# Kernel tuning notes

Hardware: AMD Instinct MI355X
Metric: run time of the kernel (lower is better)

## Reference

```python
import jax, jax.numpy as jnp
import numpy as np

B, S, E = 2, 2048, 4096
HQ, HKV, D = 32, 8, 128
WINDOW = 1024
SOFT_CAP = 50.0
Q_PRE_ATTN = 128.0
TT_SCALE = 0.1
TT_FLOOR = 8192.0
EPS = 1e-6
ROPE_BASE = 10000.0


def l2norm(x):
    return x * jax.lax.rsqrt(jnp.mean(x * x, axis=-1, keepdims=True) + EPS)


def apply_rope(x, pos):
    # x: [B,S,H,D]; half-split rotary, base 10000
    half = x.shape[-1] // 2
    freq = ROPE_BASE ** (-jnp.arange(half, dtype=jnp.float32) * 2.0 / x.shape[-1])  # [half]
    angle = pos.astype(jnp.float32)[:, None] * freq[None, :]                         # [S,half]
    cos = jnp.cos(angle)[None, :, None, :]
    sin = jnp.sin(angle)[None, :, None, :]
    x1, x2 = x[..., :half], x[..., half:]
    return jnp.concatenate([x1 * cos - x2 * sin, x2 * cos + x1 * sin], axis=-1)


def setup_inputs() -> dict:
    key = jax.random.key(0)
    ks = jax.random.split(key, 5)
    sc = 0.02
    return {
        "x": jax.random.normal(ks[0], (B, S, E), jnp.float32),
        "Wq": jax.random.normal(ks[1], (E, HQ, D), jnp.float32) * sc,
        "Wk": jax.random.normal(ks[2], (E, HKV, D), jnp.float32) * sc,
        "Wv": jax.random.normal(ks[3], (E, HKV, D), jnp.float32) * sc,
        "Wo": jax.random.normal(ks[4], (HQ, D, E), jnp.float32) * sc,
    }


def reference(x, Wq, Wk, Wv, Wo):
    pos = jnp.arange(S)
    # QKV projections
    q = jnp.einsum('bse,ehd->bshd', x, Wq)   # [B,S,HQ,D]
    k = jnp.einsum('bse,ehd->bshd', x, Wk)   # [B,S,HKV,D]
    v = jnp.einsum('bse,ehd->bshd', x, Wv)   # [B,S,HKV,D]
    # QK norm (L2Norm) then RoPE
    q = apply_rope(l2norm(q), pos)
    k = apply_rope(l2norm(k), pos)
    # query pre-attention scaling
    q = q * (Q_PRE_ATTN ** -0.5)
    # temperature tuning: per-position scale
    attn_scale = jnp.log(jnp.floor((pos.astype(jnp.float32) + 1.0) / TT_FLOOR) + 1.0) * TT_SCALE + 1.0
    q = q * attn_scale[None, :, None, None]
    # GQA: expand kv heads
    g = HQ // HKV
    k_r = jnp.repeat(k, g, axis=2)           # [B,S,HQ,D]
    v_r = jnp.repeat(v, g, axis=2)
    logits = jnp.einsum('bihd,bjhd->bhij', q, k_r).astype(jnp.float32)
    # tanh soft cap
    logits = SOFT_CAP * jnp.tanh(logits / SOFT_CAP)
    # causal + sliding window mask: j <= i and i - j < WINDOW
    i = pos[:, None]
    j = pos[None, :]
    mask = (j <= i) & ((i - j) < WINDOW)     # [S,S]
    logits = jnp.where(mask[None, None], logits, jnp.float32(-1e30))
    probs = jax.nn.softmax(logits, axis=-1)
    out = jnp.einsum('bhij,bjhd->bihd', probs, v_r)  # [B,S,HQ,D]
    return jnp.einsum('bihd,hde->bie', out, Wo)      # [B,S,E]
```

## Files before the change

### kernel.cpp

```cpp
#include <hip/hip_runtime.h>


typedef unsigned short u16;
typedef unsigned int   u32;
typedef __bf16 bf16x8 __attribute__((ext_vector_type(8)));
typedef float  f32x4  __attribute__((ext_vector_type(4)));

typedef __attribute__((address_space(1))) void* gas_ptr;
typedef __attribute__((address_space(3))) void* las_ptr;

__device__ __forceinline__ void load_lds16(const void* g, void* l) {
  __builtin_amdgcn_global_load_lds((gas_ptr)g, (las_ptr)l, 16, 0, 0);
}

__device__ __forceinline__ u16 f2bf(float f) {
  u32 u = __builtin_bit_cast(u32, f);
  u += 0x7fffu + ((u >> 16) & 1u);
  return (u16)(u >> 16);
}
__device__ __forceinline__ float bf2f(u16 h) {
  u32 u = ((u32)h) << 16;
  return __builtin_bit_cast(float, u);
}
__device__ __forceinline__ u32 pack_trunc(float a, float b) {
  return (__builtin_bit_cast(u32, a) >> 16) | (__builtin_bit_cast(u32, b) & 0xffff0000u);
}

__global__ __launch_bounds__(256) void cast_f32_bf16(const float* __restrict__ src,
                                                     u16* __restrict__ dst) {
  size_t i = ((size_t)blockIdx.x * 256 + threadIdx.x) * 8;
  float4 a = *(const float4*)(src + i);
  float4 b = *(const float4*)(src + i + 4);
  uint4 o;
  o.x = (u32)f2bf(a.x) | ((u32)f2bf(a.y) << 16);
  o.y = (u32)f2bf(a.z) | ((u32)f2bf(a.w) << 16);
  o.z = (u32)f2bf(b.x) | ((u32)f2bf(b.y) << 16);
  o.w = (u32)f2bf(b.z) | ((u32)f2bf(b.w) << 16);
  *(uint4*)(dst + i) = o;
}

__global__ __launch_bounds__(256) void transpose_cast_f32_bf16(
    const float* __restrict__ src, u16* __restrict__ dst, int R, int C) {
  __shared__ float tile[32][33];
  const int tx = threadIdx.x & 31, ty = threadIdx.x >> 5;
  const int r0 = blockIdx.y * 32, c0 = blockIdx.x * 32;
#pragma unroll
  for (int i = 0; i < 4; ++i)
    tile[ty + i * 8][tx] = src[(size_t)(r0 + ty + i * 8) * C + (c0 + tx)];
  __syncthreads();
#pragma unroll
  for (int i = 0; i < 4; ++i)
    dst[(size_t)(c0 + ty + i * 8) * R + (r0 + tx)] = f2bf(tile[tx][ty + i * 8]);
}

__global__ __launch_bounds__(256) void transpose_v(const u16* __restrict__ src,
                                                   u16* __restrict__ dst) {
  __shared__ u16 tile[32][34];
  const int plane = blockIdx.z;
  const u16* s = src + (size_t)plane * 2048 * 128;
  u16* d = dst + (size_t)plane * 2048 * 128;
  const int tx = threadIdx.x & 31, ty = threadIdx.x >> 5;
  const int r0 = blockIdx.x * 32, c0 = blockIdx.y * 32;
#pragma unroll
  for (int i = 0; i < 4; ++i)
    tile[ty + i * 8][tx] = s[(size_t)(r0 + ty + i * 8) * 128 + (c0 + tx)];
  __syncthreads();
#pragma unroll
  for (int i = 0; i < 4; ++i)
    d[(size_t)(c0 + ty + i * 8) * 2048 + (r0 + tx)] = tile[tx][ty + i * 8];
}

template <int OUT_BF16>
__global__ __launch_bounds__(256) void gemm_bt(const u16* __restrict__ A,
                                               const u16* __restrict__ Bt,
                                               void* __restrict__ Cout,
                                               int M, int N, int K) {
  __shared__ __align__(16) u16 As[128 * 32];
  __shared__ __align__(16) u16 Bs[128 * 32];
  const int t = threadIdx.x;
  const int lane = t & 63, w = t >> 6;
  const int c = lane & 15, quad = lane >> 4;
  const int m0 = blockIdx.y * 128, n0 = blockIdx.x * 128;
  const int wm = (w >> 1) * 64, wn = (w & 1) * 64;
  const int srow = lane >> 2;
  const int sch = ((lane & 3) ^ ((lane >> 3) & 3)) * 8;

  f32x4 acc[4][4];
#pragma unroll
  for (int i = 0; i < 4; ++i)
#pragma unroll
    for (int j = 0; j < 4; ++j)
#pragma unroll
      for (int r = 0; r < 4; ++r) acc[i][j][r] = 0.0f;

  const u16* Ab = A + (size_t)(m0 + w * 16 + srow) * K + sch;
  const u16* Bb = Bt + (size_t)(n0 + w * 16 + srow) * K + sch;
  const size_t row64 = (size_t)64 * K;
  u16* AsW = &As[(w * 16) * 32];
  u16* AsW2 = &As[(64 + w * 16) * 32];
  u16* BsW = &Bs[(w * 16) * 32];
  u16* BsW2 = &Bs[(64 + w * 16) * 32];

  for (int k0 = 0; k0 < K; k0 += 32) {
    __syncthreads();
    load_lds16(Ab + k0, AsW);
    load_lds16(Ab + row64 + k0, AsW2);
    load_lds16(Bb + k0, BsW);
    load_lds16(Bb + row64 + k0, BsW2);
    __syncthreads();
    bf16x8 af[4], bfr[4];
#pragma unroll
    for (int i = 0; i < 4; ++i) {
      const int row = wm + i * 16 + c;
      af[i] = *(const bf16x8*)&As[row * 32 + (quad ^ ((row >> 1) & 3)) * 8];
    }
#pragma unroll
    for (int j = 0; j < 4; ++j) {
      const int row = wn + j * 16 + c;
      bfr[j] = *(const bf16x8*)&Bs[row * 32 + (quad ^ ((row >> 1) & 3)) * 8];
    }
#pragma unroll
    for (int i = 0; i < 4; ++i)
#pragma unroll
      for (int j = 0; j < 4; ++j)
        acc[i][j] = __builtin_amdgcn_mfma_f32_16x16x32_bf16(af[i], bfr[j], acc[i][j], 0, 0, 0);
  }

#pragma unroll
  for (int i = 0; i < 4; ++i) {
#pragma unroll
    for (int j = 0; j < 4; ++j) {
      const int col = n0 + wn + j * 16 + c;
#pragma unroll
      for (int r = 0; r < 4; ++r) {
        const int row = m0 + wm + i * 16 + quad * 4 + r;
        if (OUT_BF16)
          ((u16*)Cout)[(size_t)row * N + col] = f2bf(acc[i][j][r]);
        else
          ((float*)Cout)[(size_t)row * N + col] = acc[i][j][r];
      }
    }
  }
}

__global__ __launch_bounds__(256) void qkv_post(const u16* __restrict__ raw,
                                                u16* __restrict__ qb,
                                                u16* __restrict__ kb,
                                                u16* __restrict__ vb) {
  const int t = threadIdx.x, lane = t & 63, w = t >> 6;
  const int idx = blockIdx.x * 4 + w;
  const int row = idx / 48, hh = idx - row * 48;
  const int b = row >> 11, pos = row & 2047;
  const u16* base = raw + (size_t)row * 6144 + hh * 128;
  const u16 r1 = base[lane], r2 = base[lane + 64];

  if (hh >= 40) {
    u16* dst = vb + ((size_t)((b * 8 + (hh - 40)) * 2048 + pos)) * 128;
    dst[lane] = r1;
    dst[lane + 64] = r2;
    return;
  }
  float v1 = bf2f(r1), v2 = bf2f(r2);
  float ss = v1 * v1 + v2 * v2;
#pragma unroll
  for (int off = 32; off >= 1; off >>= 1) ss += __shfl_xor(ss, off);
  const float rn = rsqrtf(ss * (1.0f / 128.0f) + 1e-6f);
  const float n1 = v1 * rn, n2 = v2 * rn;
  const float fr = exp2f(-(float)lane * 0.20762050593046f);
  const float ang = (float)pos * fr;
  float sn, cs;
  sincosf(ang, &sn, &cs);
  float o1 = n1 * cs - n2 * sn;
  float o2 = n2 * cs + n1 * sn;
  u16* dst;
  if (hh < 32) {
    const float as_ = logf(floorf((float)(pos + 1) * (1.0f / 8192.0f)) + 1.0f) * 0.1f + 1.0f;
    const float sc = 0.088388347648318447f * as_;
    o1 *= sc;
    o2 *= sc;
    dst = qb + ((size_t)((b * 32 + hh) * 2048 + pos)) * 128;
  } else {
    dst = kb + ((size_t)((b * 8 + (hh - 32)) * 2048 + pos)) * 128;
  }
  dst[lane] = f2bf(o1);
  dst[lane + 64] = f2bf(o2);
}

__global__ __launch_bounds__(256, 4) void attn_fwd(const u16* __restrict__ qb,
                                                   const u16* __restrict__ kb,
                                                   const u16* __restrict__ vtb,
                                                   u16* __restrict__ attn) {
  __shared__ __align__(16) u16 Ks[64 * 128];
  __shared__ __align__(16) u16 VTs[128 * 64];
  __shared__ __align__(16) u16 Ps[4][16 * 64];

  const int t = threadIdx.x, lane = t & 63, w = t >> 6;
  const int c = lane & 15, quad = lane >> 4;
  const int q0 = blockIdx.x * 64;
  const int bh = blockIdx.y;
  const int b = bh >> 5, hq = bh & 31;
  const int kvp = b * 8 + (hq >> 2);
  const u16* qp = qb + (size_t)bh * (2048 * 128);
  const u16* kp = kb + (size_t)kvp * (2048 * 128);
  const u16* vp = vtb + (size_t)kvp * (128 * 2048);
  u16* Psw = &Ps[w][0];

  bf16x8 qf[4];
  {
    const u16* qrow = qp + (size_t)(q0 + w * 16 + c) * 128 + quad * 8;
#pragma unroll
    for (int ks = 0; ks < 4; ++ks) qf[ks] = *(const bf16x8*)(qrow + ks * 32);
  }

  f32x4 oacc[8];
#pragma unroll
  for (int j = 0; j < 8; ++j)
#pragma unroll
    for (int r = 0; r < 4; ++r) oacc[j][r] = 0.0f;
  float lsum = 0.0f;

  const int i_glob = q0 + w * 16 + c;

  int t0 = q0 - 1023;
  if (t0 < 0) t0 = 0;
  t0 = (t0 >> 6) << 6;

  for (int kv0 = t0; kv0 <= q0; kv0 += 64) {
    __syncthreads();
    {
      const int row_in = lane >> 4, ch = lane & 15;
#pragma unroll
      for (int i = 0; i < 4; ++i) {
        const int row = w * 4 + i * 16 + row_in;
        const int g = ch ^ (row & 15);
        load_lds16(kp + (size_t)(kv0 + row) * 128 + g * 8, &Ks[(w * 4 + i * 16) * 128]);
      }
      const int drow = lane >> 3, ch8 = lane & 7;
#pragma unroll
      for (int i = 0; i < 4; ++i) {
        const int dd = w * 8 + i * 32 + drow;
        const int g = ch8 ^ (dd & 7);
        load_lds16(vp + (size_t)dd * 2048 + kv0 + g * 8, &VTs[(w * 8 + i * 32) * 64]);
      }
    }
    __syncthreads();

    f32x4 sacc[4];
#pragma unroll
    for (int im = 0; im < 4; ++im)
#pragma unroll
      for (int r = 0; r < 4; ++r) sacc[im][r] = 0.0f;

#pragma unroll
    for (int ks = 0; ks < 4; ++ks) {
#pragma unroll
      for (int im = 0; im < 4; ++im) {
        const int key = im * 16 + c;
        const int ch = (ks * 4 + quad) ^ c;
        const bf16x8 af = *(const bf16x8*)&Ks[key * 128 + ch * 8];
        sacc[im] = __builtin_amdgcn_mfma_f32_16x16x32_bf16(af, qf[ks], sacc[im], 0, 0, 0);
      }
    }

    const bool need_mask = (kv0 == q0) || (q0 - kv0 >= 961);
#pragma unroll
    for (int im = 0; im < 4; ++im) {
      float pv[4];
#pragma unroll
      for (int r = 0; r < 4; ++r) {
        const float s = sacc[im][r];
        const float u = s * s;
        const float cap = s * (1.0f + u * (-1.3333333e-4f + u * 2.1333333e-8f));
        pv[r] = __expf(cap);
      }
      if (need_mask) {
        const int j_base = kv0 + im * 16 + quad * 4;
#pragma unroll
        for (int r = 0; r < 4; ++r) {
          const int j_glob = j_base + r;
          if (!((j_glob <= i_glob) && (i_glob - j_glob < 1024))) pv[r] = 0.0f;
        }
      }
      lsum += (pv[0] + pv[1]) + (pv[2] + pv[3]);
      uint2 pk;
      pk.x = pack_trunc(pv[0], pv[1]);
      pk.y = pack_trunc(pv[2], pv[3]);
      *(uint2*)&Psw[c * 64 + ((im * 2 + (quad >> 1)) ^ (c & 7)) * 8 + (quad & 1) * 4] = pk;
    }

#pragma unroll
    for (int ks = 0; ks < 2; ++ks) {
      const bf16x8 pf = *(const bf16x8*)&Psw[c * 64 + ((ks * 4 + quad) ^ (c & 7)) * 8];
#pragma unroll
      for (int jn = 0; jn < 8; ++jn) {
        const int dd = jn * 16 + c;
        const int ch = (ks * 4 + quad) ^ (c & 7);
        const bf16x8 vf = *(const bf16x8*)&VTs[dd * 64 + ch * 8];
        oacc[jn] = __builtin_amdgcn_mfma_f32_16x16x32_bf16(pf, vf, oacc[jn], 0, 0, 0);
      }
    }
  }

  float lt = lsum;
  lt += __shfl_xor(lt, 16);
  lt += __shfl_xor(lt, 32);
  float rl[4];
#pragma unroll
  for (int r = 0; r < 4; ++r)
    rl[r] = __builtin_amdgcn_rcpf(__shfl(lt, quad * 4 + r));

  const size_t obase = ((size_t)(b * 2048 + q0 + w * 16)) * 4096 + hq * 128;
#pragma unroll
  for (int jn = 0; jn < 8; ++jn) {
#pragma unroll
    for (int r = 0; r < 4; ++r) {
      const int q_in = quad * 4 + r;
      attn[obase + (size_t)q_in * 4096 + jn * 16 + c] = f2bf(oacc[jn][r] * rl[r]);
    }
  }
}

extern "C" void kernel_launch(void* const* d_in, const int* in_sizes, int n_in,
                              void* d_out, int out_size, void* d_ws, size_t ws_size,
                              hipStream_t stream) {
  (void)in_sizes; (void)n_in; (void)out_size; (void)ws_size;
  const float* x  = (const float*)d_in[0];
  const float* Wq = (const float*)d_in[1];
  const float* Wk = (const float*)d_in[2];
  const float* Wv = (const float*)d_in[3];
  const float* Wo = (const float*)d_in[4];
  float* out = (float*)d_out;
  char* ws = (char*)d_ws;

  u16* xb    = (u16*)(ws + 0);
  u16* vtb   = (u16*)(ws + 0);
  u16* WqkvT = (u16*)(ws + 33554432ULL);
  u16* qb    = (u16*)(ws + 33554432ULL);
  u16* kb    = (u16*)(ws + 67108864ULL);
  u16* vb    = (u16*)(ws + 75497472ULL);
  u16* WoT   = (u16*)(ws + 83886080ULL);
  u16* qkvr  = (u16*)(ws + 117440512ULL);
  u16* attnb = (u16*)(ws + 117440512ULL);

  cast_f32_bf16<<<8192, 256, 0, stream>>>(x, xb);
  transpose_cast_f32_bf16<<<dim3(128, 128), 256, 0, stream>>>(Wq, WqkvT, 4096, 4096);
  transpose_cast_f32_bf16<<<dim3(32, 128), 256, 0, stream>>>(Wk, WqkvT + (size_t)4096 * 4096, 4096, 1024);
  transpose_cast_f32_bf16<<<dim3(32, 128), 256, 0, stream>>>(Wv, WqkvT + (size_t)5120 * 4096, 4096, 1024);
  transpose_cast_f32_bf16<<<dim3(128, 128), 256, 0, stream>>>(Wo, WoT, 4096, 4096);

  gemm_bt<1><<<dim3(48, 32), 256, 0, stream>>>(xb, WqkvT, (void*)qkvr, 4096, 6144, 4096);
  qkv_post<<<49152, 256, 0, stream>>>(qkvr, qb, kb, vb);
  transpose_v<<<dim3(64, 4, 16), 256, 0, stream>>>(vb, vtb);
  attn_fwd<<<dim3(32, 64), 256, 0, stream>>>(qb, kb, vtb, attnb);
  gemm_bt<0><<<dim3(32, 32), 256, 0, stream>>>(attnb, WoT, (void*)out, 4096, 4096, 4096);
}
```

Measured before the change: 830.7 us.

## Replace GEMM with 256x256-tile double-buffered pipelined kernel and block swizzle

Replaces the simple 128x128, 256-thread GEMM with a 512-thread kernel that computes 256x256 tiles with K-step 64. The 128 KB LDS is double-buffered, and async global-to-LDS loads are interleaved with MFMA phases under explicit barriers, vmcnt waits and s_setprio. It also remaps block indices so neighbouring blocks share operand tiles in cache. The aim is to hide memory latency and raise MFMA utilisation for the QKV and output projections. The cost is much higher register and LDS pressure, a hand-tuned schedule that is fragile, and a grid with few blocks (384 and 256) relative to the CU count.

```diff
diff --git a/kernel.cpp b/kernel.cpp
--- a/kernel.cpp
+++ b/kernel.cpp
@@ -70,77 +70,175 @@
     d[(size_t)(c0 + ty + i * 8) * 2048 + (r0 + tx)] = tile[tx][ty + i * 8];
 }
 
+
+template <int MB>
+__device__ __forceinline__ void mm16(f32x4 (&acc)[8][4], const bf16x8 (&af)[4],
+                                     const bf16x8 (&bf)[4]) {
+#pragma unroll
+  for (int ii = 0; ii < 4; ++ii)
+#pragma unroll
+    for (int nf = 0; nf < 4; ++nf)
+      acc[MB + ii][nf] =
+          __builtin_amdgcn_mfma_f32_16x16x32_bf16(af[ii], bf[nf], acc[MB + ii][nf], 0, 0, 0);
+}
+
 template <int OUT_BF16>
-__global__ __launch_bounds__(256) void gemm_bt(const u16* __restrict__ A,
-                                               const u16* __restrict__ Bt,
-                                               void* __restrict__ Cout,
-                                               int M, int N, int K) {
-  __shared__ __align__(16) u16 As[128 * 32];
-  __shared__ __align__(16) u16 Bs[128 * 32];
-  const int t = threadIdx.x;
-  const int lane = t & 63, w = t >> 6;
-  const int c = lane & 15, quad = lane >> 4;
-  const int m0 = blockIdx.y * 128, n0 = blockIdx.x * 128;
-  const int wm = (w >> 1) * 64, wn = (w & 1) * 64;
-  const int srow = lane >> 2;
-  const int sch = ((lane & 3) ^ ((lane >> 3) & 3)) * 8;
-
-  f32x4 acc[4][4];
-#pragma unroll
-  for (int i = 0; i < 4; ++i)
-#pragma unroll
-    for (int j = 0; j < 4; ++j)
-#pragma unroll
-      for (int r = 0; r < 4; ++r) acc[i][j][r] = 0.0f;
-
-  const u16* Ab = A + (size_t)(m0 + w * 16 + srow) * K + sch;
-  const u16* Bb = Bt + (size_t)(n0 + w * 16 + srow) * K + sch;
-  const size_t row64 = (size_t)64 * K;
-  u16* AsW = &As[(w * 16) * 32];
-  u16* AsW2 = &As[(64 + w * 16) * 32];
-  u16* BsW = &Bs[(w * 16) * 32];
-  u16* BsW2 = &Bs[(64 + w * 16) * 32];
-
-  for (int k0 = 0; k0 < K; k0 += 32) {
-    __syncthreads();
-    load_lds16(Ab + k0, AsW);
-    load_lds16(Ab + row64 + k0, AsW2);
-    load_lds16(Bb + k0, BsW);
-    load_lds16(Bb + row64 + k0, BsW2);
-    __syncthreads();
-    bf16x8 af[4], bfr[4];
-#pragma unroll
-    for (int i = 0; i < 4; ++i) {
-      const int row = wm + i * 16 + c;
-      af[i] = *(const bf16x8*)&As[row * 32 + (quad ^ ((row >> 1) & 3)) * 8];
-    }
-#pragma unroll
-    for (int j = 0; j < 4; ++j) {
-      const int row = wn + j * 16 + c;
-      bfr[j] = *(const bf16x8*)&Bs[row * 32 + (quad ^ ((row >> 1) & 3)) * 8];
-    }
-#pragma unroll
-    for (int i = 0; i < 4; ++i)
-#pragma unroll
-      for (int j = 0; j < 4; ++j)
-        acc[i][j] = __builtin_amdgcn_mfma_f32_16x16x32_bf16(af[i], bfr[j], acc[i][j], 0, 0, 0);
-  }
-
-#pragma unroll
-  for (int i = 0; i < 4; ++i) {
-#pragma unroll
-    for (int j = 0; j < 4; ++j) {
-      const int col = n0 + wn + j * 16 + c;
+__global__ __launch_bounds__(512, 2) void gemm256(const u16* __restrict__ A,
+                                                  const u16* __restrict__ Bt,
+                                                  void* __restrict__ Cout,
+                                                  int N, int K, int ntx) {
+  __shared__ __align__(16) u16 lds[65536];
+  const int t = threadIdx.x, lane = t & 63, w = t >> 6;
+  const int c = lane & 15, q = lane >> 4;
+  const int wm = w >> 2, wn = w & 3;
+
+  const int cpx = (int)gridDim.x >> 3;
+  const int swz = ((int)blockIdx.x & 7) * cpx + ((int)blockIdx.x >> 3);
+  const int bx = swz % ntx, by = swz / ntx;
+  const int m0 = by << 8, n0 = bx << 8;
+
+  u32 aoff[2][2], boff[2][2];
+#pragma unroll
+  for (int h = 0; h < 2; ++h)
+#pragma unroll
+    for (int j = 0; j < 2; ++j) {
+      const int rowS = w * 16 + j * 8 + (lane >> 3);
+      const int colE = ((lane & 7) ^ (rowS & 7)) * 8;
+      aoff[h][j] = (u32)(m0 + h * 128 + rowS) * (u32)K + (u32)colE;
+      boff[h][j] = (u32)(n0 + h * 128 + rowS) * (u32)K + (u32)colE;
+    }
+  const u32 stW = (u32)w * 1024u;
+
+  const u32 sl0 = (u32)((q ^ (c & 7)) * 8);
+  const u32 aR = (u32)(wm * 8192 + c * 64) + sl0;
+  const u32 bR = (u32)(16384 + (wn >> 1) * 8192 + (wn & 1) * 4096 + c * 64) + sl0;
+
+  f32x4 acc[8][4];
+#pragma unroll
+  for (int i2 = 0; i2 < 8; ++i2)
+#pragma unroll
+    for (int j2 = 0; j2 < 4; ++j2) acc[i2][j2] = (f32x4){0.f, 0.f, 0.f, 0.f};
+
+  const int nt = K >> 6;
+
+#define STG_A(bb, hh, kt)                                                \
+  do {                                                                   \
+    u16* d_ = &lds[(bb) * 32768u + (hh) * 8192u + stW];                  \
+    load_lds16(A + (aoff[hh][0] + (u32)(kt) * 64u), d_);                 \
+    load_lds16(A + (aoff[hh][1] + (u32)(kt) * 64u), d_ + 512);           \
+  } while (0)
+#define STG_B(bb, hh, kt)                                                \
+  do {                                                                   \
+    u16* d_ = &lds[(bb) * 32768u + 16384u + (hh) * 8192u + stW];         \
+    load_lds16(Bt + (boff[hh][0] + (u32)(kt) * 64u), d_);                \
+    load_lds16(Bt + (boff[hh][1] + (u32)(kt) * 64u), d_ + 512);          \
+  } while (0)
+#define RD4(dst, base)                                                   \
+  do {                                                                   \
+    const u16* p_ = &lds[(base)];                                        \
+    dst[0] = *(const bf16x8*)(p_);                                       \
+    dst[1] = *(const bf16x8*)(p_ + 1024);                                \
+    dst[2] = *(const bf16x8*)(p_ + 2048);                                \
+    dst[3] = *(const bf16x8*)(p_ + 3072);                                \
+  } while (0)
+#define BAR __builtin_amdgcn_s_barrier()
+#define LGKM0 asm volatile("s_waitcnt lgkmcnt(0)" ::: "memory")
+#define VM6 asm volatile("s_waitcnt vmcnt(6)" ::: "memory")
+#define PRIO1 __builtin_amdgcn_s_setprio(1)
+#define PRIO0 __builtin_amdgcn_s_setprio(0)
+
+  STG_B(0, 0, 0);
+  STG_B(0, 1, 0);
+  STG_A(0, 0, 0);
+  STG_A(0, 1, 0);
+  STG_B(1, 0, 1);
+  STG_B(1, 1, 1);
+  STG_A(1, 0, 1);
+  VM6;
+  BAR;
+
+  bf16x8 Bf0[4], Bf1[4], Af0[4], Af1[4];
+
+  for (int i = 0; i < (nt >> 1); ++i) {
+    const int tb = 2 * i + 1;
+    int t2 = 2 * i + 2; if (t2 >= nt) t2 -= nt;
+    int t3 = 2 * i + 3; if (t3 >= nt) t3 -= nt;
+
+    RD4(Bf0, bR);
+    RD4(Bf1, bR ^ 32u);
+    RD4(Af0, aR);
+    STG_A(1, 1, tb);
+    BAR; LGKM0;
+    PRIO1; mm16<0>(acc, Af0, Bf0); PRIO0;
+    BAR;
+    RD4(Af1, aR + 4096u);
+    STG_B(0, 0, t2);
+    BAR; LGKM0;
+    PRIO1; mm16<4>(acc, Af1, Bf0); PRIO0;
+    BAR;
+    RD4(Af0, aR ^ 32u);
+    RD4(Af1, (aR + 4096u) ^ 32u);
+    STG_B(0, 1, t2);
+    BAR; LGKM0;
+    PRIO1; mm16<0>(acc, Af0, Bf1); PRIO0;
+    BAR;
+    STG_A(0, 0, t2);
+    VM6;
+    BAR;
+    PRIO1; mm16<4>(acc, Af1, Bf1); PRIO0;
+    BAR;
+
+    RD4(Bf0, 32768u + bR);
+    RD4(Bf1, (32768u + bR) ^ 32u);
+    RD4(Af0, 32768u + aR);
+    STG_A(0, 1, t2);
+    BAR; LGKM0;
+    PRIO1; mm16<0>(acc, Af0, Bf0); PRIO0;
+    BAR;
+    RD4(Af1, 32768u + aR + 4096u);
+    STG_B(1, 0, t3);
+    BAR; LGKM0;
+    PRIO1; mm16<4>(acc, Af1, Bf0); PRIO0;
+    BAR;
+    RD4(Af0, (32768u + aR) ^ 32u);
+    RD4(Af1, (32768u + aR + 4096u) ^ 32u);
+    STG_B(1, 1, t3);
+    BAR; LGKM0;
+    PRIO1; mm16<0>(acc, Af0, Bf1); PRIO0;
+    BAR;
+    STG_A(1, 0, t3);
+    VM6;
+    BAR;
+    PRIO1; mm16<4>(acc, Af1, Bf1); PRIO0;
+    BAR;
+  }
+
+  asm volatile("s_waitcnt vmcnt(0)" ::: "memory");
+
+#undef STG_A
+#undef STG_B
+#undef RD4
+#undef BAR
+#undef LGKM0
+#undef VM6
+#undef PRIO1
+#undef PRIO0
+
+  const int rb0 = m0 + wm * 128 + q * 4;
+  const int cb0 = n0 + wn * 64 + c;
+#pragma unroll
+  for (int mf = 0; mf < 8; ++mf)
+#pragma unroll
+    for (int nf = 0; nf < 4; ++nf) {
+      const size_t base = (size_t)(rb0 + mf * 16) * N + (cb0 + nf * 16);
 #pragma unroll
       for (int r = 0; r < 4; ++r) {
-        const int row = m0 + wm + i * 16 + quad * 4 + r;
         if (OUT_BF16)
-          ((u16*)Cout)[(size_t)row * N + col] = f2bf(acc[i][j][r]);
+          ((u16*)Cout)[base + (size_t)r * N] = f2bf(acc[mf][nf][r]);
         else
-          ((float*)Cout)[(size_t)row * N + col] = acc[i][j][r];
-      }
-    }
-  }
+          ((float*)Cout)[base + (size_t)r * N] = acc[mf][nf][r];
+      }
+    }
 }
 
 __global__ __launch_bounds__(256) void qkv_post(const u16* __restrict__ raw,
@@ -348,9 +446,9 @@
   transpose_cast_f32_bf16<<<dim3(32, 128), 256, 0, stream>>>(Wv, WqkvT + (size_t)5120 * 4096, 4096, 1024);
   transpose_cast_f32_bf16<<<dim3(128, 128), 256, 0, stream>>>(Wo, WoT, 4096, 4096);
 
-  gemm_bt<1><<<dim3(48, 32), 256, 0, stream>>>(xb, WqkvT, (void*)qkvr, 4096, 6144, 4096);
+  gemm256<1><<<dim3(384), 512, 0, stream>>>(xb, WqkvT, (void*)qkvr, 6144, 4096, 24);
   qkv_post<<<49152, 256, 0, stream>>>(qkvr, qb, kb, vb);
   transpose_v<<<dim3(64, 4, 16), 256, 0, stream>>>(vb, vtb);
   attn_fwd<<<dim3(32, 64), 256, 0, stream>>>(qb, kb, vtb, attnb);
-  gemm_bt<0><<<dim3(32, 32), 256, 0, stream>>>(attnb, WoT, (void*)out, 4096, 4096, 4096);
-}
+  gemm256<0><<<dim3(256), 512, 0, stream>>>(attnb, WoT, (void*)out, 4096, 4096, 16);
+}
```

After: 710.1 us. 14.5% less time.
